# Performance work log

Hardware: AMD Instinct MI355X
Metric: run time of the kernel (lower is better)

## Reference

```python
import jax, jax.numpy as jnp
import numpy as np

DIM = 2048
N_HEADS = 16
HEAD_DIM = 128
KV_HEADS = 1
ROPE_BASE = 10000.0


def _rope_tables(T, dim, dtype):
    inv_freq = 1.0 / (ROPE_BASE ** (jnp.arange(0, dim, 2, dtype=jnp.float32) / dim))
    t = jnp.arange(T, dtype=jnp.float32)
    freqs = jnp.einsum('i,j->ij', t, inv_freq)          # [T, dim/2]
    emb = jnp.concatenate([freqs, freqs], axis=-1)      # [T, dim]
    cos = jnp.cos(emb)[None, None, :, :].astype(dtype)  # [1,1,T,dim]
    sin = jnp.sin(emb)[None, None, :, :].astype(dtype)
    return cos, sin


def _rotate_half(x):
    x1, x2 = jnp.split(x, 2, axis=-1)
    return jnp.concatenate([-x2, x1], axis=-1)


def setup_inputs() -> dict:
    key = jax.random.key(0)
    k1, k2, k3, k4, k5 = jax.random.split(key, 5)
    B, T = 2, 2048
    x = jax.random.normal(k1, (B, T, DIM), dtype=jnp.float32)
    # additive causal mask: 0 on/below diagonal, -1e9 above
    causal = jnp.triu(jnp.full((T, T), -1e9, dtype=jnp.float32), k=1)
    attn_mask = causal[None, None, :, :]
    s = 1.0 / np.sqrt(DIM)
    wq = jax.random.normal(k2, (DIM, N_HEADS * HEAD_DIM), dtype=jnp.float32) * s
    wk = jax.random.normal(k3, (DIM, KV_HEADS * HEAD_DIM), dtype=jnp.float32) * s
    wv = jax.random.normal(k4, (DIM, KV_HEADS * HEAD_DIM), dtype=jnp.float32) * s
    wo = jax.random.normal(k5, (N_HEADS * HEAD_DIM, DIM), dtype=jnp.float32) * s
    return {"x": x, "attn_mask": attn_mask, "wq": wq, "wk": wk, "wv": wv, "wo": wo}


def reference(x, attn_mask, wq, wk, wv, wo):
    B, T, C = x.shape
    q = (x @ wq).reshape(B, T, N_HEADS, HEAD_DIM).transpose(0, 2, 1, 3)   # [B,H,T,d]
    k = (x @ wk).reshape(B, T, KV_HEADS, HEAD_DIM).transpose(0, 2, 1, 3)  # [B,1,T,d]
    v = (x @ wv).reshape(B, T, KV_HEADS, HEAD_DIM).transpose(0, 2, 1, 3)  # [B,1,T,d]
    cos, sin = _rope_tables(T, HEAD_DIM, x.dtype)
    q = q * cos + _rotate_half(q) * sin
    k = k * cos + _rotate_half(k) * sin
    # KV head broadcasts over the H dim inside matmul (MQA expand path)
    att = jnp.matmul(q, k.swapaxes(-1, -2)) / np.sqrt(HEAD_DIM)          # [B,H,T,T]
    att = att + attn_mask
    w = jax.nn.softmax(att, axis=-1)
    y = jnp.matmul(w, v)                                                  # [B,H,T,d]
    y = y.transpose(0, 2, 1, 3).reshape(B, T, N_HEADS * HEAD_DIM)
    y = y @ wo
    k_exp = jnp.broadcast_to(k, (B, N_HEADS, T, HEAD_DIM))
    v_exp = jnp.broadcast_to(v, (B, N_HEADS, T, HEAD_DIM))
    return y, k_exp, v_exp
```

## Files before the change

### kernel.cpp

```cpp
#include <hip/hip_runtime.h>
#include <hip/hip_bf16.h>
#include <cstdint>
#include <cstddef>

#define B_SZ   2
#define T_SEQ  2048
#define C_DIM  2048
#define NH     16
#define HD     128

typedef __attribute__((ext_vector_type(8))) short s8v;
typedef __attribute__((ext_vector_type(4))) float f32x4;

typedef __attribute__((address_space(3))) char lds_char;
typedef __attribute__((address_space(1))) const char glob_char;

#define QSCALE 0.12751887f

__device__ __forceinline__ unsigned short f2bf(float f) {
    union { float f; uint32_t i; } v; v.f = f;
    uint32_t r = (v.i + 0x7FFFu + ((v.i >> 16) & 1u)) >> 16;
    return (unsigned short)r;
}

__device__ __forceinline__ unsigned int cvt2_bf16(float a, float b) {
    unsigned int w;
    asm("v_cvt_pk_bf16_f32 %0, %1, %2" : "=v"(w) : "v"(a), "v"(b));
    return w;
}

__global__ __launch_bounds__(256) void k_prep(
        const float* __restrict__ x, unsigned short* __restrict__ xb,
        float* __restrict__ cosT, float* __restrict__ sinT,
        float* __restrict__ cosT2, float* __restrict__ sinT2,
        const float* __restrict__ wq, const float* __restrict__ wk,
        const float* __restrict__ wv, const float* __restrict__ wo,
        unsigned short* __restrict__ wT, unsigned short* __restrict__ woT) {
    __shared__ unsigned short tile[64][66];
    int blk = blockIdx.x;
    int tid = threadIdx.x;

    if (blk < 2048) {
        int i = blk * 256 + tid;
        const int n4 = 4096 * 2048 / 4;
        const int stride = 2048 * 256;
        for (; i < n4; i += stride) {
            float4 v = reinterpret_cast<const float4*>(x)[i];
            ushort4 o;
            o.x = f2bf(v.x); o.y = f2bf(v.y); o.z = f2bf(v.z); o.w = f2bf(v.w);
            reinterpret_cast<ushort4*>(xb)[i] = o;
        }
        return;
    }
    blk -= 2048;
    if (blk < 512) {
        int idx = blk * 256 + tid;
        int t = idx >> 6, i = idx & 63;
        float inv = powf(10000.0f, -(float)i / 64.0f);
        float ang = (float)t * inv;
        float c = cosf(ang), s = sinf(ang);
        cosT[idx] = c;  sinT[idx] = s;
        cosT2[i * T_SEQ + t] = c;  sinT2[i * T_SEQ + t] = s;
        return;
    }
    blk -= 512;

    const float* in; unsigned short* out; int C, ldo, bx, by;
    if (blk < 1024) {
        in = wq; out = wT; C = 2048; ldo = 2048;
        bx = blk & 31; by = blk >> 5;
    } else if (blk < 1088) {
        int l = blk - 1024;
        in = wk; out = wT + (size_t)2048 * 2048; C = 128; ldo = 2048;
        bx = l & 1; by = l >> 1;
    } else if (blk < 1152) {
        int l = blk - 1088;
        in = wv; out = wT + (size_t)2176 * 2048; C = 128; ldo = 2048;
        bx = l & 1; by = l >> 1;
    } else {
        int l = blk - 1152;
        in = wo; out = woT; C = 2048; ldo = 2048;
        bx = l & 31; by = l >> 5;
    }
    int x0 = bx * 64, y0 = by * 64;
    int tx = tid & 63, ty = tid >> 6;
#pragma unroll
    for (int j = 0; j < 16; ++j) {
        int r = y0 + ty + j * 4;
        tile[ty + j * 4][tx] = f2bf(in[(size_t)r * C + x0 + tx]);
    }
    __syncthreads();
#pragma unroll
    for (int j = 0; j < 16; ++j) {
        int orow = x0 + ty + j * 4;
        out[(size_t)orow * ldo + y0 + tx] = tile[tx][ty + j * 4];
    }
}

#define BM 128
#define BN 128
#define BK 64

__global__ __launch_bounds__(256) void k_gemm_bt(
        const unsigned short* __restrict__ A,
        const unsigned short* __restrict__ Bt,
        float* __restrict__ C, int M, int N, int K, int ldc, int gx) {
    __shared__ char smem[BM * BK * 2 + BN * BK * 2];
    char* As = smem;
    char* Bs = smem + BM * BK * 2;
    int tid = threadIdx.x, lane = tid & 63, wid = tid >> 6;
    int nwg = gridDim.x, cpx = nwg >> 3;
    int orig = blockIdx.x;
    int wg = (orig & 7) * cpx + (orig >> 3);
    int bx = wg % gx, by = wg / gx;
    int m0 = by * BM, n0 = bx * BN;
    int wr = wid >> 1, wc = wid & 1;

    f32x4 acc[4][4] = {};

    int srow = wid * 32 + (lane >> 3);
    int cp = lane & 7;

    for (int k0 = 0; k0 < K; k0 += BK) {
#pragma unroll
        for (int i = 0; i < 4; ++i) {
            int row = srow + i * 8;
            int c = cp ^ (row & 7);
            const unsigned short* ga = A + (size_t)(m0 + row) * K + k0 + c * 8;
            const unsigned short* gb = Bt + (size_t)(n0 + row) * K + k0 + c * 8;
            __builtin_amdgcn_global_load_lds((glob_char*)ga,
                (lds_char*)(As + wid * 4096 + i * 1024), 16, 0, 0);
            __builtin_amdgcn_global_load_lds((glob_char*)gb,
                (lds_char*)(Bs + wid * 4096 + i * 1024), 16, 0, 0);
        }
        __syncthreads();

#pragma unroll
        for (int kc = 0; kc < 2; ++kc) {
            s8v af[4], bfr[4];
#pragma unroll
            for (int mi = 0; mi < 4; ++mi) {
                int row = wr * 64 + mi * 16 + (lane & 15);
                int slot = (kc * 4 + (lane >> 4)) ^ (row & 7);
                af[mi] = *reinterpret_cast<const s8v*>(As + row * 128 + slot * 16);
            }
#pragma unroll
            for (int ni = 0; ni < 4; ++ni) {
                int row = wc * 64 + ni * 16 + (lane & 15);
                int slot = (kc * 4 + (lane >> 4)) ^ (row & 7);
                bfr[ni] = *reinterpret_cast<const s8v*>(Bs + row * 128 + slot * 16);
            }
#pragma unroll
            for (int mi = 0; mi < 4; ++mi)
#pragma unroll
                for (int ni = 0; ni < 4; ++ni)
                    acc[mi][ni] = __builtin_amdgcn_mfma_f32_16x16x32_bf16(
                        af[mi], bfr[ni], acc[mi][ni], 0, 0, 0);
        }
        __syncthreads();
    }

#pragma unroll
    for (int mi = 0; mi < 4; ++mi) {
        int row = m0 + wr * 64 + mi * 16 + ((lane >> 4) << 2);
#pragma unroll
        for (int ni = 0; ni < 4; ++ni) {
            int col = n0 + wc * 64 + ni * 16 + (lane & 15);
            float* cp2 = C + (size_t)row * ldc + col;
#pragma unroll
            for (int r = 0; r < 4; ++r)
                cp2[(size_t)r * ldc] = acc[mi][ni][r];
        }
    }
}

__global__ __launch_bounds__(256) void k_gemm_qkv(
        const unsigned short* __restrict__ A,
        const unsigned short* __restrict__ Bt,
        const float* __restrict__ cosT2,
        const float* __restrict__ sinT2,
        unsigned short* __restrict__ qB,
        float* __restrict__ qkvKV) {
    const int GX = 18, K = 2048;
    __shared__ char smem[34816];
    char* As = smem;
    char* Bs = smem + BM * BK * 2;
    int tid = threadIdx.x, lane = tid & 63, wid = tid >> 6;
    int nwg = gridDim.x, cpx = nwg >> 3;
    int orig = blockIdx.x;
    int wg = (orig & 7) * cpx + (orig >> 3);
    int bx = wg % GX, by = wg / GX;
    int m0 = by * BM, n0 = bx * BN;
    int l15 = lane & 15, l4 = lane >> 4;
    int wr = wid >> 1, wc = wid & 1;

    f32x4 acc[4][4] = {};

    int srow = wid * 32 + (lane >> 3);
    int cp = lane & 7;

    for (int k0 = 0; k0 < K; k0 += BK) {
#pragma unroll
        for (int i = 0; i < 4; ++i) {
            int row = srow + i * 8;
            int c = cp ^ (row & 7);
            const unsigned short* ga = A + (size_t)(m0 + row) * K + k0 + c * 8;
            const unsigned short* gb = Bt + (size_t)(n0 + row) * K + k0 + c * 8;
            __builtin_amdgcn_global_load_lds((glob_char*)ga,
                (lds_char*)(As + wid * 4096 + i * 1024), 16, 0, 0);
            __builtin_amdgcn_global_load_lds((glob_char*)gb,
                (lds_char*)(Bs + wid * 4096 + i * 1024), 16, 0, 0);
        }
        __syncthreads();

#pragma unroll
        for (int kc = 0; kc < 2; ++kc) {
            s8v af[4], bfr[4];
#pragma unroll
            for (int mi = 0; mi < 4; ++mi) {
                int row = wr * 64 + mi * 16 + l15;
                int slot = (kc * 4 + l4) ^ (row & 7);
                af[mi] = *reinterpret_cast<const s8v*>(As + row * 128 + slot * 16);
            }
#pragma unroll
            for (int ni = 0; ni < 4; ++ni) {
                int row = wc * 64 + ni * 16 + l15;
                int slot = (kc * 4 + l4) ^ (row & 7);
                bfr[ni] = *reinterpret_cast<const s8v*>(Bs + row * 128 + slot * 16);
            }
#pragma unroll
            for (int mi = 0; mi < 4; ++mi)
#pragma unroll
                for (int ni = 0; ni < 4; ++ni)
                    acc[mi][ni] = __builtin_amdgcn_mfma_f32_16x16x32_bf16(
                        af[mi], bfr[ni], acc[mi][ni], 0, 0, 0);
        }
        __syncthreads();
    }

    if (bx < 16) {
        float* xch = reinterpret_cast<float*>(smem);
        if (wc == 1) {
            float* base = xch + ((size_t)wr * 64 + lane) * 68;
#pragma unroll
            for (int mi = 0; mi < 4; ++mi)
#pragma unroll
                for (int ni = 0; ni < 4; ++ni)
                    *reinterpret_cast<f32x4*>(base + mi * 16 + ni * 4) =
                        acc[mi][ni];
        }
        __syncthreads();
        if (wc == 0) {
            int b = m0 >> 11, h = bx;
            const float* pbase = xch + ((size_t)wr * 64 + lane) * 68;
#pragma unroll
            for (int mi = 0; mi < 4; ++mi) {
                int t0 = ((m0 & (T_SEQ - 1)) + wr * 64 + mi * 16 + l4 * 4);
#pragma unroll
                for (int ni = 0; ni < 4; ++ni) {
                    int d = ni * 16 + l15;
                    float4 c4 = *reinterpret_cast<const float4*>(
                        cosT2 + (size_t)d * T_SEQ + t0);
                    float4 s4 = *reinterpret_cast<const float4*>(
                        sinT2 + (size_t)d * T_SEQ + t0);
                    f32x4 px = *reinterpret_cast<const f32x4*>(
                        pbase + mi * 16 + ni * 4);
#pragma unroll
                    for (int r = 0; r < 4; ++r) {
                        float x1 = acc[mi][ni][r];
                        float x2 = px[r];
                        float cc = (&c4.x)[r], ss = (&s4.x)[r];
                        float o1 = (x1 * cc - x2 * ss) * QSCALE;
                        float o2 = (x2 * cc + x1 * ss) * QSCALE;
                        size_t qoff = ((size_t)(b * NH + h) * T_SEQ + t0 + r)
                                      * HD + 2 * d;
                        *reinterpret_cast<unsigned int*>(qB + qoff) =
                            cvt2_bf16(o1, o2);
                    }
                }
            }
        }
    } else {
        int colb = (bx - 16) * 128;
#pragma unroll
        for (int mi = 0; mi < 4; ++mi) {
            int row = m0 + wr * 64 + mi * 16 + l4 * 4;
#pragma unroll
            for (int ni = 0; ni < 4; ++ni) {
                int col = colb + wc * 64 + ni * 16 + l15;
                float* cp2 = qkvKV + (size_t)row * 256 + col;
#pragma unroll
                for (int r = 0; r < 4; ++r)
                    cp2[(size_t)r * 256] = acc[mi][ni][r];
            }
        }
    }
}

__global__ __launch_bounds__(192) void k_kv_transform(
                               const float* __restrict__ qkvKV,
                               const float* __restrict__ cosT,
                               const float* __restrict__ sinT,
                               unsigned short* __restrict__ kB,
                               unsigned short* __restrict__ vT,
                               float* __restrict__ kexp,
                               float* __restrict__ vexp) {
    int bt = blockIdx.x;
    int b = bt >> 11, t = bt & 2047;
    int tid = threadIdx.x;
    const float* base = qkvKV + (size_t)bt * 256;

    if (tid < 64) {
        int d = tid;
        float c = cosT[t * 64 + d], s = sinT[t * 64 + d];
        float k1 = base[d], k2 = base[d + 64];
        float o1 = k1 * c - k2 * s;
        float o2 = k2 * c + k1 * s;
        size_t koff = ((size_t)b * T_SEQ + t) * HD + 2 * d;
        *reinterpret_cast<unsigned int*>(kB + koff) = cvt2_bf16(o1, o2);
#pragma unroll
        for (int h = 0; h < NH; ++h) {
            size_t eoff = ((size_t)(b * NH + h) * T_SEQ + t) * HD + d;
            kexp[eoff] = o1;
            kexp[eoff + 64] = o2;
        }
    } else {
        int d = tid - 64;
        float v = base[128 + d];
        vT[((size_t)b * HD + d) * T_SEQ + t] = f2bf(v);
#pragma unroll
        for (int h = 0; h < NH; ++h)
            vexp[((size_t)(b * NH + h) * T_SEQ + t) * HD + d] = v;
    }
}

__global__ __launch_bounds__(256, 3) void k_flash_attn(
        const unsigned short* __restrict__ qB,
        const unsigned short* __restrict__ kB,
        const unsigned short* __restrict__ vT,
        unsigned short* __restrict__ yattn) {
    __shared__ char smem[49152];
    int tid = threadIdx.x, lane = tid & 63, wvid = tid >> 6;
    int l15 = lane & 15, l4 = lane >> 4;
    int blk = blockIdx.x;
    int bh = blk & 31;
    int b = bh >> 4, h = bh & 15;
    int g = blk >> 5;
    int a = g & 7, qq = g >> 3;
    int u = (qq == 0) ? (31 - a) : (qq == 1) ? (16 + a)
          : (qq == 2) ? (15 - a) : a;
    int qrow0 = u * 64 + wvid * 16;

    const unsigned short* kbB   = kB + (size_t)b * T_SEQ * HD;
    const unsigned short* vbase = vT + (size_t)b * HD * T_SEQ;

    const unsigned short* qbase =
        qB + ((size_t)(b * NH + h) * T_SEQ + qrow0) * HD;
    s8v aq[4];
#pragma unroll
    for (int kc = 0; kc < 4; ++kc)
        aq[kc] = *reinterpret_cast<const s8v*>(
            qbase + (size_t)l15 * HD + kc * 32 + l4 * 8);

    float m = -3e38f, l = 0.f;
    f32x4 o[8] = {};

    int NT = 2 * u + 2;

    auto stage = [&](int buf, int t) {
        int kv0 = t * 32;
        char* kdst = smem + buf * 16384;
        char* vdst = smem + buf * 16384 + 8192;
#pragma unroll
        for (int j = 0; j < 2; ++j) {
            int n = j * 256 + tid;
            int row = n >> 4, ch = n & 15;
            const unsigned short* src =
                kbB + (size_t)(kv0 + row) * HD + (ch ^ (row & 7)) * 8;
            __builtin_amdgcn_global_load_lds((glob_char*)src,
                (lds_char*)(kdst + j * 4096 + wvid * 1024), 16, 0, 0);
        }
#pragma unroll
        for (int j = 0; j < 2; ++j) {
            int n = j * 256 + tid;
            int row = n >> 2, ch = n & 3;
            const unsigned short* src =
                vbase + (size_t)row * T_SEQ + kv0 + (ch ^ ((row >> 1) & 3)) * 8;
            __builtin_amdgcn_global_load_lds((glob_char*)src,
                (lds_char*)(vdst + j * 4096 + wvid * 1024), 16, 0, 0);
        }
    };

    stage(0, 0);
    stage(1, 1);
    asm volatile("s_waitcnt vmcnt(4)" ::: "memory");
    __builtin_amdgcn_s_barrier();
    __builtin_amdgcn_sched_barrier(0);

    int cur = 0;
    for (int t = 0; t < NT; ++t) {
        int nb = cur + 2; if (nb >= 3) nb -= 3;
        if (t + 2 < NT) stage(nb, t + 2);
        int kv0 = t * 32;
        const char* Kc = smem + cur * 16384;
        const char* Vc = smem + cur * 16384 + 8192;
        int act = (kv0 <= qrow0 + 15);

        if (act) {
            f32x4 sfr[2] = {};
            __builtin_amdgcn_s_setprio(1);
#pragma unroll
            for (int kc = 0; kc < 4; ++kc) {
                s8v kf[2];
#pragma unroll
                for (int n = 0; n < 2; ++n) {
                    int row = n * 16 + l15;
                    int byte = row * 256 +
                        ((kc * 64 + l4 * 16) ^ ((row & 7) << 4));
                    kf[n] = *reinterpret_cast<const s8v*>(Kc + byte);
                }
#pragma unroll
                for (int n = 0; n < 2; ++n)
                    sfr[n] = __builtin_amdgcn_mfma_f32_16x16x32_bf16(
                        kf[n], aq[kc], sfr[n], 0, 0, 0);
            }
            __builtin_amdgcn_s_setprio(0);

            if (kv0 + 31 > qrow0) {
                int qa = qrow0 + l15;
#pragma unroll
                for (int n = 0; n < 2; ++n)
#pragma unroll
                    for (int r = 0; r < 4; ++r) {
                        int kv = kv0 + n * 16 + l4 * 4 + r;
                        if (kv > qa) sfr[n][r] = -1e9f;
                    }
            }

            float pm = sfr[0][0];
#pragma unroll
            for (int r = 1; r < 4; ++r) pm = fmaxf(pm, sfr[0][r]);
#pragma unroll
            for (int r = 0; r < 4; ++r) pm = fmaxf(pm, sfr[1][r]);
            pm = fmaxf(pm, __shfl_xor(pm, 16));
            pm = fmaxf(pm, __shfl_xor(pm, 32));
            if (!__all(pm <= m + 8.0f)) {
                float mn = fmaxf(m, pm);
                float al = exp2f(m - mn);
                l *= al;
#pragma unroll
                for (int ds = 0; ds < 8; ++ds)
#pragma unroll
                    for (int r = 0; r < 4; ++r) o[ds][r] *= al;
                m = mn;
            }
#pragma unroll
            for (int n = 0; n < 2; ++n)
#pragma unroll
                for (int r = 0; r < 4; ++r) {
                    float p = exp2f(sfr[n][r] - m);
                    sfr[n][r] = p;
                    l += p;
                }

            unsigned int a0 = cvt2_bf16(sfr[0][0], sfr[0][1]);
            unsigned int a1 = cvt2_bf16(sfr[0][2], sfr[0][3]);
            unsigned int b0 = cvt2_bf16(sfr[1][0], sfr[1][1]);
            unsigned int b1 = cvt2_bf16(sfr[1][2], sfr[1][3]);
            int srcE = (lane & 15) | ((lane & 16) << 1);
            int srcO = srcE + 16;
            unsigned int ae0 = __shfl(a0, srcE), ae1 = __shfl(a1, srcE);
            unsigned int be0 = __shfl(b0, srcE), be1 = __shfl(b1, srcE);
            unsigned int ao0 = __shfl(a0, srcO), ao1 = __shfl(a1, srcO);
            unsigned int bo0 = __shfl(b0, srcO), bo1 = __shfl(b1, srcO);
            bool lo = (lane & 32) == 0;
            union { unsigned int u[4]; s8v v; } pf;
            pf.u[0] = lo ? ae0 : be0;
            pf.u[1] = lo ? ae1 : be1;
            pf.u[2] = lo ? ao0 : bo0;
            pf.u[3] = lo ? ao1 : bo1;

            __builtin_amdgcn_s_setprio(1);
#pragma unroll
            for (int ds = 0; ds < 8; ++ds) {
                int vrow = ds * 16 + l15;
                int vbyte = vrow * 64 + ((l4 * 16) ^ (((vrow >> 1) & 3) << 4));
                s8v bv = *reinterpret_cast<const s8v*>(Vc + vbyte);
                o[ds] = __builtin_amdgcn_mfma_f32_16x16x32_bf16(
                    bv, pf.v, o[ds], 0, 0, 0);
            }
            __builtin_amdgcn_s_setprio(0);
        }

        if (t + 2 < NT) {
            asm volatile("s_waitcnt vmcnt(4) lgkmcnt(0)" ::: "memory");
        } else {
            asm volatile("s_waitcnt vmcnt(0) lgkmcnt(0)" ::: "memory");
        }
        __builtin_amdgcn_s_barrier();
        __builtin_amdgcn_sched_barrier(0);
        cur = (cur == 2) ? 0 : cur + 1;
    }

    l += __shfl_xor(l, 16);
    l += __shfl_xor(l, 32);
    float inv = 1.0f / l;
    size_t rowoff = ((size_t)b * T_SEQ + qrow0 + l15) * C_DIM + h * HD;
#pragma unroll
    for (int ds = 0; ds < 8; ++ds) {
        uint2 w;
        w.x = cvt2_bf16(o[ds][0] * inv, o[ds][1] * inv);
        w.y = cvt2_bf16(o[ds][2] * inv, o[ds][3] * inv);
        *reinterpret_cast<uint2*>(yattn + rowoff + ds * 16 + l4 * 4) = w;
    }
}

extern "C" void kernel_launch(void* const* d_in, const int* in_sizes, int n_in,
                              void* d_out, int out_size, void* d_ws, size_t ws_size,
                              hipStream_t stream) {
    const float* x  = (const float*)d_in[0];
    const float* wq = (const float*)d_in[2];
    const float* wk = (const float*)d_in[3];
    const float* wv = (const float*)d_in[4];
    const float* wo = (const float*)d_in[5];

    char* ws = (char*)d_ws;
    size_t off = 0;
    auto alloc = [&](size_t bytes) -> void* {
        void* p = ws + off;
        off += (bytes + 255) & ~(size_t)255;
        return p;
    };
    unsigned short* xb    = (unsigned short*)alloc((size_t)4096 * 2048 * 2);
    unsigned short* wT    = (unsigned short*)alloc((size_t)2304 * 2048 * 2);
    unsigned short* woT   = (unsigned short*)alloc((size_t)2048 * 2048 * 2);
    float*          qkvKV = (float*)alloc((size_t)4096 * 256 * 4);
    float*          cosT  = (float*)alloc((size_t)2048 * 64 * 4);
    float*          sinT  = (float*)alloc((size_t)2048 * 64 * 4);
    float*          cosT2 = (float*)alloc((size_t)64 * 2048 * 4);
    float*          sinT2 = (float*)alloc((size_t)64 * 2048 * 4);
    unsigned short* qB    = (unsigned short*)alloc((size_t)2 * 16 * 2048 * 128 * 2);
    unsigned short* kB    = (unsigned short*)alloc((size_t)2 * 2048 * 128 * 2);
    unsigned short* vT    = (unsigned short*)alloc((size_t)2 * 128 * 2048 * 2);
    unsigned short* yattn = (unsigned short*)alloc((size_t)4096 * 2048 * 2);

    float* y_out = (float*)d_out;
    float* kexp  = y_out + (size_t)2 * 2048 * 2048;
    float* vexp  = kexp + (size_t)2 * 16 * 2048 * 128;

    k_prep<<<4736, 256, 0, stream>>>(x, xb, cosT, sinT, cosT2, sinT2,
                                     wq, wk, wv, wo, wT, woT);
    k_gemm_qkv<<<576, 256, 0, stream>>>(xb, wT, cosT2, sinT2, qB, qkvKV);
    k_kv_transform<<<4096, 192, 0, stream>>>(qkvKV, cosT, sinT, kB, vT, kexp, vexp);
    k_flash_attn<<<1024, 256, 0, stream>>>(qB, kB, vT, yattn);
    k_gemm_bt<<<512, 256, 0, stream>>>(
        yattn, woT, y_out, 4096, 2048, 2048, 2048, 16);
}
```

Before: 229.4 us.

## Process two query heads per flash-attention block to reuse shared K/V tiles

```diff
diff --git a/kernel.cpp b/kernel.cpp
--- a/kernel.cpp
+++ b/kernel.cpp
@@ -343,9 +343,9 @@
     int tid = threadIdx.x, lane = tid & 63, wvid = tid >> 6;
     int l15 = lane & 15, l4 = lane >> 4;
     int blk = blockIdx.x;
-    int bh = blk & 31;
-    int b = bh >> 4, h = bh & 15;
-    int g = blk >> 5;
+    int bp = blk & 15;
+    int b = bp >> 3, hp = bp & 7;
+    int g = blk >> 4;
     int a = g & 7, qq = g >> 3;
     int u = (qq == 0) ? (31 - a) : (qq == 1) ? (16 + a)
           : (qq == 2) ? (15 - a) : a;
@@ -354,16 +354,19 @@
     const unsigned short* kbB   = kB + (size_t)b * T_SEQ * HD;
     const unsigned short* vbase = vT + (size_t)b * HD * T_SEQ;
 
-    const unsigned short* qbase =
-        qB + ((size_t)(b * NH + h) * T_SEQ + qrow0) * HD;
-    s8v aq[4];
-#pragma unroll
-    for (int kc = 0; kc < 4; ++kc)
-        aq[kc] = *reinterpret_cast<const s8v*>(
-            qbase + (size_t)l15 * HD + kc * 32 + l4 * 8);
-
-    float m = -3e38f, l = 0.f;
-    f32x4 o[8] = {};
+    s8v aq[2][4];
+#pragma unroll
+    for (int hh = 0; hh < 2; ++hh) {
+        const unsigned short* qbase =
+            qB + ((size_t)(b * NH + 2 * hp + hh) * T_SEQ + qrow0) * HD;
+#pragma unroll
+        for (int kc = 0; kc < 4; ++kc)
+            aq[hh][kc] = *reinterpret_cast<const s8v*>(
+                qbase + (size_t)l15 * HD + kc * 32 + l4 * 8);
+    }
+
+    float m[2] = {-3e38f, -3e38f}, l[2] = {0.f, 0.f};
+    f32x4 o[2][8] = {};
 
     int NT = 2 * u + 2;
 
@@ -407,7 +410,7 @@
         int act = (kv0 <= qrow0 + 15);
 
         if (act) {
-            f32x4 sfr[2] = {};
+            f32x4 sfr[2][2] = {};
             __builtin_amdgcn_s_setprio(1);
 #pragma unroll
             for (int kc = 0; kc < 4; ++kc) {
@@ -420,65 +423,69 @@
                     kf[n] = *reinterpret_cast<const s8v*>(Kc + byte);
                 }
 #pragma unroll
+                for (int hh = 0; hh < 2; ++hh)
+#pragma unroll
+                    for (int n = 0; n < 2; ++n)
+                        sfr[hh][n] = __builtin_amdgcn_mfma_f32_16x16x32_bf16(
+                            kf[n], aq[hh][kc], sfr[hh][n], 0, 0, 0);
+            }
+            __builtin_amdgcn_s_setprio(0);
+
+            union { unsigned int u[4]; s8v v; } pf[2];
+#pragma unroll
+            for (int hh = 0; hh < 2; ++hh) {
+                if (kv0 + 31 > qrow0) {
+                    int qa = qrow0 + l15;
+#pragma unroll
+                    for (int n = 0; n < 2; ++n)
+#pragma unroll
+                        for (int r = 0; r < 4; ++r) {
+                            int kv = kv0 + n * 16 + l4 * 4 + r;
+                            if (kv > qa) sfr[hh][n][r] = -1e9f;
+                        }
+                }
+                float pm = sfr[hh][0][0];
+#pragma unroll
+                for (int r = 1; r < 4; ++r) pm = fmaxf(pm, sfr[hh][0][r]);
+#pragma unroll
+                for (int r = 0; r < 4; ++r) pm = fmaxf(pm, sfr[hh][1][r]);
+                pm = fmaxf(pm, __shfl_xor(pm, 16));
+                pm = fmaxf(pm, __shfl_xor(pm, 32));
+                if (!__all(pm <= m[hh] + 8.0f)) {
+                    float mn = fmaxf(m[hh], pm);
+                    float al = exp2f(m[hh] - mn);
+                    l[hh] *= al;
+#pragma unroll
+                    for (int ds = 0; ds < 8; ++ds)
+#pragma unroll
+                        for (int r = 0; r < 4; ++r) o[hh][ds][r] *= al;
+                    m[hh] = mn;
+                }
+#pragma unroll
                 for (int n = 0; n < 2; ++n)
-                    sfr[n] = __builtin_amdgcn_mfma_f32_16x16x32_bf16(
-                        kf[n], aq[kc], sfr[n], 0, 0, 0);
-            }
-            __builtin_amdgcn_s_setprio(0);
-
-            if (kv0 + 31 > qrow0) {
-                int qa = qrow0 + l15;
-#pragma unroll
-                for (int n = 0; n < 2; ++n)
 #pragma unroll
                     for (int r = 0; r < 4; ++r) {
-                        int kv = kv0 + n * 16 + l4 * 4 + r;
-                        if (kv > qa) sfr[n][r] = -1e9f;
+                        float p = exp2f(sfr[hh][n][r] - m[hh]);
+                        sfr[hh][n][r] = p;
+                        l[hh] += p;
                     }
-            }
-
-            float pm = sfr[0][0];
-#pragma unroll
-            for (int r = 1; r < 4; ++r) pm = fmaxf(pm, sfr[0][r]);
-#pragma unroll
-            for (int r = 0; r < 4; ++r) pm = fmaxf(pm, sfr[1][r]);
-            pm = fmaxf(pm, __shfl_xor(pm, 16));
-            pm = fmaxf(pm, __shfl_xor(pm, 32));
-            if (!__all(pm <= m + 8.0f)) {
-                float mn = fmaxf(m, pm);
-                float al = exp2f(m - mn);
-                l *= al;
-#pragma unroll
-                for (int ds = 0; ds < 8; ++ds)
-#pragma unroll
-                    for (int r = 0; r < 4; ++r) o[ds][r] *= al;
-                m = mn;
-            }
-#pragma unroll
-            for (int n = 0; n < 2; ++n)
-#pragma unroll
-                for (int r = 0; r < 4; ++r) {
-                    float p = exp2f(sfr[n][r] - m);
-                    sfr[n][r] = p;
-                    l += p;
-                }
-
-            unsigned int a0 = cvt2_bf16(sfr[0][0], sfr[0][1]);
-            unsigned int a1 = cvt2_bf16(sfr[0][2], sfr[0][3]);
-            unsigned int b0 = cvt2_bf16(sfr[1][0], sfr[1][1]);
-            unsigned int b1 = cvt2_bf16(sfr[1][2], sfr[1][3]);
-            int srcE = (lane & 15) | ((lane & 16) << 1);
-            int srcO = srcE + 16;
-            unsigned int ae0 = __shfl(a0, srcE), ae1 = __shfl(a1, srcE);
-            unsigned int be0 = __shfl(b0, srcE), be1 = __shfl(b1, srcE);
-            unsigned int ao0 = __shfl(a0, srcO), ao1 = __shfl(a1, srcO);
-            unsigned int bo0 = __shfl(b0, srcO), bo1 = __shfl(b1, srcO);
-            bool lo = (lane & 32) == 0;
-            union { unsigned int u[4]; s8v v; } pf;
-            pf.u[0] = lo ? ae0 : be0;
-            pf.u[1] = lo ? ae1 : be1;
-            pf.u[2] = lo ? ao0 : bo0;
-            pf.u[3] = lo ? ao1 : bo1;
+
+                unsigned int a0 = cvt2_bf16(sfr[hh][0][0], sfr[hh][0][1]);
+                unsigned int a1 = cvt2_bf16(sfr[hh][0][2], sfr[hh][0][3]);
+                unsigned int b0 = cvt2_bf16(sfr[hh][1][0], sfr[hh][1][1]);
+                unsigned int b1 = cvt2_bf16(sfr[hh][1][2], sfr[hh][1][3]);
+                int srcE = (lane & 15) | ((lane & 16) << 1);
+                int srcO = srcE + 16;
+                unsigned int ae0 = __shfl(a0, srcE), ae1 = __shfl(a1, srcE);
+                unsigned int be0 = __shfl(b0, srcE), be1 = __shfl(b1, srcE);
+                unsigned int ao0 = __shfl(a0, srcO), ao1 = __shfl(a1, srcO);
+                unsigned int bo0 = __shfl(b0, srcO), bo1 = __shfl(b1, srcO);
+                bool lo = (lane & 32) == 0;
+                pf[hh].u[0] = lo ? ae0 : be0;
+                pf[hh].u[1] = lo ? ae1 : be1;
+                pf[hh].u[2] = lo ? ao0 : bo0;
+                pf[hh].u[3] = lo ? ao1 : bo1;
+            }
 
             __builtin_amdgcn_s_setprio(1);
 #pragma unroll
@@ -486,8 +493,10 @@
                 int vrow = ds * 16 + l15;
                 int vbyte = vrow * 64 + ((l4 * 16) ^ (((vrow >> 1) & 3) << 4));
                 s8v bv = *reinterpret_cast<const s8v*>(Vc + vbyte);
-                o[ds] = __builtin_amdgcn_mfma_f32_16x16x32_bf16(
-                    bv, pf.v, o[ds], 0, 0, 0);
+                o[0][ds] = __builtin_amdgcn_mfma_f32_16x16x32_bf16(
+                    bv, pf[0].v, o[0][ds], 0, 0, 0);
+                o[1][ds] = __builtin_amdgcn_mfma_f32_16x16x32_bf16(
+                    bv, pf[1].v, o[1][ds], 0, 0, 0);
             }
             __builtin_amdgcn_s_setprio(0);
         }
@@ -502,16 +511,21 @@
         cur = (cur == 2) ? 0 : cur + 1;
     }
 
-    l += __shfl_xor(l, 16);
-    l += __shfl_xor(l, 32);
-    float inv = 1.0f / l;
-    size_t rowoff = ((size_t)b * T_SEQ + qrow0 + l15) * C_DIM + h * HD;
-#pragma unroll
-    for (int ds = 0; ds < 8; ++ds) {
-        uint2 w;
-        w.x = cvt2_bf16(o[ds][0] * inv, o[ds][1] * inv);
-        w.y = cvt2_bf16(o[ds][2] * inv, o[ds][3] * inv);
-        *reinterpret_cast<uint2*>(yattn + rowoff + ds * 16 + l4 * 4) = w;
+#pragma unroll
+    for (int hh = 0; hh < 2; ++hh) {
+        float lv = l[hh];
+        lv += __shfl_xor(lv, 16);
+        lv += __shfl_xor(lv, 32);
+        float inv = 1.0f / lv;
+        size_t rowoff = ((size_t)b * T_SEQ + qrow0 + l15) * C_DIM
+                        + (2 * hp + hh) * HD;
+#pragma unroll
+        for (int ds = 0; ds < 8; ++ds) {
+            uint2 w;
+            w.x = cvt2_bf16(o[hh][ds][0] * inv, o[hh][ds][1] * inv);
+            w.y = cvt2_bf16(o[hh][ds][2] * inv, o[hh][ds][3] * inv);
+            *reinterpret_cast<uint2*>(yattn + rowoff + ds * 16 + l4 * 4) = w;
+        }
     }
 }
 
@@ -552,7 +566,7 @@
                                      wq, wk, wv, wo, wT, woT);
     k_gemm_qkv<<<576, 256, 0, stream>>>(xb, wT, cosT2, sinT2, qB, qkvKV);
     k_kv_transform<<<4096, 192, 0, stream>>>(qkvKV, cosT, sinT, kB, vT, kexp, vexp);
-    k_flash_attn<<<1024, 256, 0, stream>>>(qB, kB, vT, yattn);
+    k_flash_attn<<<512, 256, 0, stream>>>(qB, kB, vT, yattn);
     k_gemm_bt<<<512, 256, 0, stream>>>(
         yattn, woT, y_out, 4096, 2048, 2048, 2048, 16);
 }
```

New measurement: 252.1 us. 1.1x slower.
